# Kernel optimization log

Hardware: AMD Instinct MI355X
Metric: run time of the kernel (lower is better)

Reference implementation:

```python
import jax, jax.numpy as jnp
import numpy as np

B, C, S, H, W = 1, 256, 64, 32, 128
BLOCKS, HEADS, DH = 2, 8, 32
SCALE = DH ** (-0.5)


def layer_norm(x, w, b, eps=1e-5):
    mu = jnp.mean(x, axis=-1, keepdims=True)
    var = jnp.var(x, axis=-1, keepdims=True)
    return (x - mu) * jax.lax.rsqrt(var + eps) * w + b


def generate_y_for_attn(y, u):
    # y: (B,C,H,W), u: (B,S,S) float -> (B, S^2, 2H, C)
    Bv, Cv, Hv, Wv = y.shape
    Sv = u.shape[1]
    uf = jnp.floor(u).reshape(Bv, Sv * Sv)
    u_left = jnp.clip(uf, 0, Wv - 1).astype(jnp.int32)
    u_right = jnp.clip(uf + 1, 0, Wv - 1).astype(jnp.int32)
    yf = y.reshape(Bv, Cv * Hv, Wv)

    def gather_w(idx):
        idxb = jnp.broadcast_to(idx[:, None, :], (Bv, Cv * Hv, Sv * Sv))
        return jnp.take_along_axis(yf, idxb, axis=2).reshape(Bv, Cv, Hv, Sv * Sv)

    ys = jnp.concatenate([gather_w(u_left), gather_w(u_right)], axis=2)  # (B,C,2H,S2)
    return ys.transpose(0, 3, 2, 1)  # (B, S2, 2H, C)


def cross_attention(x, y, p, i):
    # x: (B,M,C), y: (B,M,N,C)
    q = layer_norm(x, p['ln_q_w'][i], p['ln_q_b'][i]) @ p['Wq'][i]        # (B,M,HD)
    k = layer_norm(y, p['ln_k_w'][i], p['ln_k_b'][i]) @ p['Wk'][i]        # (B,M,N,HD)
    v = layer_norm(y, p['ln_v_w'][i], p['ln_v_b'][i]) @ p['Wv'][i]        # (B,M,N,HD)
    Bv, M, _ = q.shape
    N = k.shape[2]
    q = q.reshape(Bv, M, HEADS, DH)
    k = k.reshape(Bv, M, N, HEADS, DH)
    v = v.reshape(Bv, M, N, HEADS, DH)
    dot = SCALE * jnp.einsum('bmhd,bmnhd->bhmn', q, k)                    # (B,H,M,N)
    attn = jax.nn.softmax(dot, axis=-1)
    a = jnp.einsum('bhmn,bmnhd->bmhd', attn, v).reshape(Bv, M, HEADS * DH)
    z = a @ p['Wproj'][i] + p['bproj'][i]
    z = layer_norm(z, p['ln_pre_w'][i], p['ln_pre_b'][i])
    h = jax.nn.gelu(z @ p['Wm1'][i] + p['bm1'][i], approximate=False)
    z = z + (h @ p['Wm2'][i] + p['bm2'][i])
    return layer_norm(z, p['ln_post_w'][i], p['ln_post_b'][i])


def setup_inputs() -> dict:
    key = jax.random.key(0)
    ks = jax.random.split(key, 16)
    std = 0.02
    inp = {
        'grd2sat': jax.random.normal(ks[0], (B, C, S, S), jnp.float32),
        'grd_x': jax.random.normal(ks[1], (B, C, H, W), jnp.float32),
        'u': jax.random.uniform(ks[2], (B, S, S), jnp.float32) * (W - 1),
        'ln_q_w': jnp.ones((BLOCKS, C)), 'ln_q_b': jnp.zeros((BLOCKS, C)),
        'ln_k_w': jnp.ones((BLOCKS, C)), 'ln_k_b': jnp.zeros((BLOCKS, C)),
        'ln_v_w': jnp.ones((BLOCKS, C)), 'ln_v_b': jnp.zeros((BLOCKS, C)),
        'Wq': std * jax.random.normal(ks[3], (BLOCKS, C, HEADS * DH)),
        'Wk': std * jax.random.normal(ks[4], (BLOCKS, C, HEADS * DH)),
        'Wv': std * jax.random.normal(ks[5], (BLOCKS, C, HEADS * DH)),
        'Wproj': std * jax.random.normal(ks[6], (BLOCKS, HEADS * DH, C)),
        'bproj': jnp.zeros((BLOCKS, C)),
        'ln_pre_w': jnp.ones((BLOCKS, C)), 'ln_pre_b': jnp.zeros((BLOCKS, C)),
        'Wm1': std * jax.random.normal(ks[7], (BLOCKS, C, 2 * C)),
        'bm1': jnp.zeros((BLOCKS, 2 * C)),
        'Wm2': std * jax.random.normal(ks[8], (BLOCKS, 2 * C, C)),
        'bm2': jnp.zeros((BLOCKS, C)),
        'ln_post_w': jnp.ones((BLOCKS, C)), 'ln_post_b': jnp.zeros((BLOCKS, C)),
    }
    return inp


def reference(grd2sat, grd_x, u, ln_q_w, ln_q_b, ln_k_w, ln_k_b, ln_v_w, ln_v_b,
              Wq, Wk, Wv, Wproj, bproj, ln_pre_w, ln_pre_b, Wm1, bm1, Wm2, bm2,
              ln_post_w, ln_post_b):
    p = dict(ln_q_w=ln_q_w, ln_q_b=ln_q_b, ln_k_w=ln_k_w, ln_k_b=ln_k_b,
             ln_v_w=ln_v_w, ln_v_b=ln_v_b, Wq=Wq, Wk=Wk, Wv=Wv, Wproj=Wproj,
             bproj=bproj, ln_pre_w=ln_pre_w, ln_pre_b=ln_pre_b, Wm1=Wm1, bm1=bm1,
             Wm2=Wm2, bm2=bm2, ln_post_w=ln_post_w, ln_post_b=ln_post_b)
    y_attn = generate_y_for_attn(grd_x, u)               # (B, S^2, 2H, C)
    x = grd2sat.reshape(B, C, S * S).transpose(0, 2, 1)  # (B, M, C)
    for i in range(BLOCKS):
        # (Swin self-attention layer omitted; cross-attention stack only.)
        x = cross_attention(x, y_attn, p, i)
    out = x.transpose(0, 2, 1).reshape(B, C, S, S)
    # L2 normalize over channel dim
    norm = jnp.sqrt(jnp.sum(out * out, axis=1, keepdims=True))
    return out / jnp.maximum(norm, 1e-12)
```

## Files before the change

kernel.cpp:

```cpp
#include <hip/hip_runtime.h>
#include <math.h>


#define C_DIM 256
#define M_DIM 4096
#define W_DIM 128
#define H_DIM 32
#define ATT_SCALE 0.17677669529663687f

typedef __attribute__((ext_vector_type(8))) short short8;
typedef __attribute__((ext_vector_type(4))) short short4v;
typedef __attribute__((ext_vector_type(4))) float floatx4;

__device__ __forceinline__ unsigned short f2bf(float f) {
    unsigned u = __float_as_uint(f);
    unsigned r = (u + 0x7fffu + ((u >> 16) & 1u)) >> 16;
    return (unsigned short)r;
}
__device__ __forceinline__ float gelu_exact(float x) {
    return 0.5f * x * (1.0f + erff(x * 0.70710678118654752f));
}

struct PrepArgs {
    const float* grd2sat; float* xcur;
    const float* grd_x;   float* yhat;
    const float* u; int* perm; int4* chunks; int* nchunks;
    const float* win[12]; unsigned short* wout[12]; const float* wlnw[12];
    int wR[12], wC[12], wbase[13];
    const float* fW[10]; const float* flnb[10]; const float* fbase[10];
    float* fout[10];
    int fN[10], fwcol[10], focol[10];
};

__global__ __launch_bounds__(256) void prep_kernel(PrepArgs a) {
    __shared__ float smemf[9024];
    int b = blockIdx.x, t = threadIdx.x;
    if (b < 256) {
        float (*tile)[65] = (float(*)[65])smemf;
        int m0 = (b & 63) << 6, c0 = (b >> 6) << 6;
        for (int it = 0; it < 16; ++it) {
            int idx = it * 256 + t;
            int co = idx >> 6, mo = idx & 63;
            tile[co][mo] = a.grd2sat[(size_t)(c0 + co) * M_DIM + m0 + mo];
        }
        __syncthreads();
        for (int it = 0; it < 16; ++it) {
            int idx = it * 256 + t;
            int mo = idx >> 6, co = idx & 63;
// ... 15 lines not shown
        __syncthreads();
        {
            int w = t & 31, part = t >> 5;
            float s = 0.f, ss = 0.f;
            for (int c = part * 32; c < part * 32 + 32; ++c) {
                float x = tile[c][w];
                s += x; ss += x * x;
            }
            ps[part][w] = s; pss[part][w] = ss;
        }
        __syncthreads();
        if (t < 32) {
            float s = 0.f, ss = 0.f;
            for (int p = 0; p < 8; ++p) { s += ps[p][t]; ss += pss[p][t]; }
            float mu = s * (1.f / 256.f);
            float var = ss * (1.f / 256.f) - mu * mu;
            mu_s[t] = mu;
            rs_s[t] = rsqrtf(var + 1e-5f);
        }
        __syncthreads();
        for (int jj = 0; jj < 32; ++jj) {
            float mu = mu_s[jj], rs = rs_s[jj];
            a.yhat[((size_t)(w0 + jj) * H_DIM + h) * C_DIM + t] =
                (tile[t][jj] - mu) * rs;
        }
    } else if (b < 1408) {
        int wI = b - 384;
        int e = 0;
        while (wI >= a.wbase[e + 1]) ++e;
        int tl = wI - a.wbase[e];
        int tilesC = a.wC[e] >> 5;
        int tr = tl / tilesC, tc = tl - tr * tilesC;
        int r0 = tr << 5, c0 = tc << 5;
        const float* in = a.win[e];
        unsigned short* out = a.wout[e];
        const float* lnw = a.wlnw[e];
        int R = a.wR[e], Cc = a.wC[e];
        float (*tile)[33] = (float(*)[33])smemf;
        int rl = t >> 3, cq = (t & 7) << 2;
        float4 v = *(const float4*)&in[(size_t)(r0 + rl) * Cc + c0 + cq];
        if (lnw) {
            float s = lnw[r0 + rl];
            v.x *= s; v.y *= s; v.z *= s; v.w *= s;
        }
        tile[rl][cq + 0] = v.x;
        tile[rl][cq + 1] = v.y;
        tile[rl][cq + 2] = v.z;
        tile[rl][cq + 3] = v.w;
        __syncthreads();
        int cl = t >> 3, rq = (t & 7) << 2;
        ushort4 o;
        o.x = f2bf(tile[rq + 0][cl]);
        o.y = f2bf(tile[rq + 1][cl]);
        o.z = f2bf(tile[rq + 2][cl]);
        o.w = f2bf(tile[rq + 3][cl]);
        *(ushort4*)&out[(size_t)(c0 + cl) * R + r0 + rq] = o;
    } else if (b < 1448) {
        int idx = b - 1408;
        int jj = idx >> 2, part = idx & 3;
        int N = a.fN[jj];
        int c = t & 63, kp = t >> 6;
        int wcol = a.fwcol[jj] + (part << 6) + c;
        const float* W = a.fW[jj];
        const float* lb = a.flnb[jj];
        float s = 0.f;
        for (int k = kp * 64; k < kp * 64 + 64; ++k)
            s += lb[k] * W[(size_t)k * N + wcol];
        smemf[(kp << 6) + c] = s;
        __syncthreads();
        if (t < 64) {
            float tot = smemf[t] + smemf[64 + t] + smemf[128 + t] + smemf[192 + t];
            int ocol = a.focol[jj] + (part << 6) + t;
            if (a.fbase[jj]) tot += a.fbase[jj][a.fwcol[jj] + (part << 6) + t];
            a.fout[jj][ocol] = tot;
        }
    } else {
        int* hist = (int*)smemf;
        int* cur = (int*)smemf + 128;
        unsigned short* wlb = (unsigned short*)((int*)smemf + 256);
        if (t < 128) hist[t] = 0;
        __syncthreads();
        for (int it = 0; it < 16; ++it) {
            int m = it * 256 + t;
            int wl = (int)floorf(a.u[m]);
            wl = max(0, min(wl, 126));
            wlb[m] = (unsigned short)wl;
            atomicAdd(&hist[wl], 1);
        }
// ... 20 lines not shown
            int pos = atomicAdd(&cur[wl], 1);
            a.perm[pos] = m;
        }
    }
}

struct GJ {
    const void* A; const unsigned short* Bt;
    const float* bias;
    void* out; unsigned short* out2;
    int K, N;
};

__device__ __forceinline__ void gemm_core_kv(const GJ& j, short (*As)[264],
                                             short (*Bs)[264], int bm, int by) {
    int t = threadIdx.x;
    int bn = by << 6;
    int wv = t >> 6, lane = t & 63;
    int mt = wv & 1, nt0 = (wv >> 1) << 1;
    int quad = lane >> 4, l16 = lane & 15;
    floatx4 acc0 = {0.f, 0.f, 0.f, 0.f};
    floatx4 acc1 = {0.f, 0.f, 0.f, 0.f};
    {
        int ar = t >> 3, cq = (t & 7) << 2;
        const float* ap = (const float*)j.A + (size_t)(bm + ar) * 256 + cq;
        float4 v[8];
#pragma unroll
        for (int g = 0; g < 8; ++g) v[g] = *(const float4*)(ap + g * 32);
#pragma unroll
        for (int g = 0; g < 8; ++g) {
            short4v o;
            o[0] = (short)f2bf(v[g].x);
            o[1] = (short)f2bf(v[g].y);
            o[2] = (short)f2bf(v[g].z);
            o[3] = (short)f2bf(v[g].w);
            *(short4v*)&As[ar][cq + g * 32] = o;
        }
    }
    {
        int br = t >> 2, cq2 = (t & 3) << 3;
        const unsigned short* bp = j.Bt + (size_t)(bn + br) * 256 + cq2;
#pragma unroll
        for (int g = 0; g < 8; ++g)
            *(short8*)&Bs[br][cq2 + g * 32] = *(const short8*)(bp + g * 32);
    }
    __syncthreads();
#pragma unroll
    for (int k0 = 0; k0 < 8; ++k0) {
        short8 aa = *(const short8*)&As[(mt << 4) + l16][(k0 << 5) + (quad << 3)];
        short8 b0 = *(const short8*)&Bs[(nt0 << 4) + l16][(k0 << 5) + (quad << 3)];
        short8 b1 =
            *(const short8*)&Bs[((nt0 + 1) << 4) + l16][(k0 << 5) + (quad << 3)];
        acc0 = __builtin_amdgcn_mfma_f32_16x16x32_bf16(aa, b0, acc0, 0, 0, 0);
        acc1 = __builtin_amdgcn_mfma_f32_16x16x32_bf16(aa, b1, acc1, 0, 0, 0);
    }
#pragma unroll
    for (int jj = 0; jj < 2; ++jj) {
        const floatx4 accv = jj ? acc1 : acc0;
        int col = bn + ((nt0 + jj) << 4) + l16;
        float bv = j.bias[col];
// ... 12 lines not shown
__global__ __launch_bounds__(256) void kv_kernel(GJ j0, GJ j1) {
    __shared__ short As[32][264];
    __shared__ short Bs[64][264];
    int bm = blockIdx.x << 5;
    if ((int)blockIdx.y < 8)
        gemm_core_kv(j0, As, Bs, bm, blockIdx.y);
    else
        gemm_core_kv(j1, As, Bs, bm, blockIdx.y - 8);
}

struct MegaArgs {
    const float* xcur;
    const int* perm; const int4* chunks; const int* nchunks;
    float* xfinal;
    const unsigned short* Wq[2]; const unsigned short* Wp[2];
    const unsigned short* Wm1[2]; const unsigned short* Wm2[2];
    const unsigned short* Ktb[2]; const unsigned short* Vtb[2];
    const float* qb[2]; const float* m1b[2];
    const float* bpj[2]; const float* bm2v[2];
    const float* pw[2]; const float* pb[2];
    const float* aw; const float* ab;
};

struct BPre { short8 b[8][2]; };

__device__ __forceinline__ void preloadB(const unsigned short* Bt, int Kstride,
                                         int koff, int colw, int l16, int quad,
                                         BPre& P) {
    const unsigned short* bp =
        Bt + (size_t)(colw + l16) * Kstride + koff + (quad << 3);
#pragma unroll
    for (int k0 = 0; k0 < 8; ++k0)
#pragma unroll
        for (int ni = 0; ni < 2; ++ni)
            P.b[k0][ni] =
                *(const short8*)(bp + (size_t)(ni << 4) * Kstride + (k0 << 5));
}

__device__ __forceinline__ void mfma32t(const short* As, int lda, const BPre& P,
                                        int l16, int quad, floatx4 acc[2][2]) {
    const short* ap = As + (size_t)l16 * lda + (quad << 3);
#pragma unroll
    for (int k0 = 0; k0 < 8; ++k0) {
        short8 a0 = *(const short8*)(ap + (k0 << 5));
        short8 a1 = *(const short8*)(ap + (size_t)16 * lda + (k0 << 5));
        acc[0][0] = __builtin_amdgcn_mfma_f32_16x16x32_bf16(a0, P.b[k0][0], acc[0][0], 0, 0, 0);
        acc[0][1] = __builtin_amdgcn_mfma_f32_16x16x32_bf16(a0, P.b[k0][1], acc[0][1], 0, 0, 0);
        acc[1][0] = __builtin_amdgcn_mfma_f32_16x16x32_bf16(a1, P.b[k0][0], acc[1][0], 0, 0, 0);
        acc[1][1] = __builtin_amdgcn_mfma_f32_16x16x32_bf16(a1, P.b[k0][1], acc[1][1], 0, 0, 0);
    }
}

#define ZACC(A) \
    { A[0][0] = (floatx4){0.f,0.f,0.f,0.f}; A[0][1] = (floatx4){0.f,0.f,0.f,0.f}; \
      A[1][0] = (floatx4){0.f,0.f,0.f,0.f}; A[1][1] = (floatx4){0.f,0.f,0.f,0.f}; }

__global__ __launch_bounds__(512) void mega_kernel(MegaArgs a) {
    __shared__ __align__(16) char smem[137856];
    short (*XH)[264] = (short(*)[264])(smem);
    short (*QR)[264] = (short(*)[264])(smem + 16896);
    short (*ZH)[264] = (short(*)[264])(smem + 33792);
    short (*AR)[264] = (short(*)[264])(smem + 50688);
    float (*Zf)[260] = (float(*)[260])(smem + 67584);
    short (*PB)[32][72] = (short(*)[32][72])(smem + 100864);
    int* gp = (int*)(smem + 137728);

    if ((int)blockIdx.x >= *a.nchunks) return;
    int4 cd = a.chunks[blockIdx.x];
    int wl = cd.x, qstart = cd.y, qcnt = cd.z;
    int t = threadIdx.x;
    if (t < 32) gp[t] = (t < qcnt) ? a.perm[qstart + t] : a.perm[qstart];
    __syncthreads();

    int wv = t >> 6, lane = t & 63, quad = lane >> 4, l16 = lane & 15;
    int colw = wv << 5;
    int r16 = t >> 4, c0 = (t & 15) << 4;

#pragma unroll 1
    for (int l = 0; l < 2; ++l) {
        BPre Pq;
        preloadB(a.Wq[l], 256, 0, colw, l16, quad, Pq);
        {
            float4 v[4];
            if (l == 0) {
                const float* xp = a.xcur + (size_t)gp[r16] * 256 + c0;
#pragma unroll
                for (int g4 = 0; g4 < 4; ++g4)
                    v[g4] = *(const float4*)(xp + (g4 << 2));
            } else {
#pragma unroll
                for (int g4 = 0; g4 < 4; ++g4)
                    v[g4] = *(const float4*)&Zf[r16][c0 + (g4 << 2)];
            }
            float s = 0.f, ss = 0.f;
#pragma unroll
            for (int g4 = 0; g4 < 4; ++g4) {
                s += v[g4].x + v[g4].y + v[g4].z + v[g4].w;
                ss += v[g4].x * v[g4].x + v[g4].y * v[g4].y + v[g4].z * v[g4].z +
                      v[g4].w * v[g4].w;
            }
#pragma unroll
            for (int o = 1; o < 16; o <<= 1) {
                s += __shfl_xor(s, o, 64);
                ss += __shfl_xor(ss, o, 64);
            }
            float mu = s * (1.f / 256.f);
            float rs = rsqrtf(ss * (1.f / 256.f) - mu * mu + 1e-5f);
#pragma unroll
            for (int g4 = 0; g4 < 4; ++g4) {
                v[g4].x = (v[g4].x - mu) * rs;
                v[g4].y = (v[g4].y - mu) * rs;
                v[g4].z = (v[g4].z - mu) * rs;
                v[g4].w = (v[g4].w - mu) * rs;
            }
            if (l == 1) {
                float s2 = 0.f, ss2 = 0.f;
#pragma unroll
                for (int g4 = 0; g4 < 4; ++g4) {
                    float4 w4 = *(const float4*)&a.aw[c0 + (g4 << 2)];
                    float4 b4 = *(const float4*)&a.ab[c0 + (g4 << 2)];
                    v[g4].x = v[g4].x * w4.x + b4.x;
                    v[g4].y = v[g4].y * w4.y + b4.y;
                    v[g4].z = v[g4].z * w4.z + b4.z;
                    v[g4].w = v[g4].w * w4.w + b4.w;
                    s2 += v[g4].x + v[g4].y + v[g4].z + v[g4].w;
                    ss2 += v[g4].x * v[g4].x + v[g4].y * v[g4].y +
                           v[g4].z * v[g4].z + v[g4].w * v[g4].w;
                }
#pragma unroll
                for (int o = 1; o < 16; o <<= 1) {
                    s2 += __shfl_xor(s2, o, 64);
                    ss2 += __shfl_xor(ss2, o, 64);
                }
                float mu2 = s2 * (1.f / 256.f);
                float rs2 = rsqrtf(ss2 * (1.f / 256.f) - mu2 * mu2 + 1e-5f);
#pragma unroll
                for (int g4 = 0; g4 < 4; ++g4) {
                    v[g4].x = (v[g4].x - mu2) * rs2;
                    v[g4].y = (v[g4].y - mu2) * rs2;
                    v[g4].z = (v[g4].z - mu2) * rs2;
                    v[g4].w = (v[g4].w - mu2) * rs2;
                }
            }
#pragma unroll
            for (int g4 = 0; g4 < 4; ++g4) {
                short4v o;
                o[0] = (short)f2bf(v[g4].x);
                o[1] = (short)f2bf(v[g4].y);
                o[2] = (short)f2bf(v[g4].z);
                o[3] = (short)f2bf(v[g4].w);
                *(short4v*)&XH[r16][c0 + (g4 << 2)] = o;
            }
        }
        __syncthreads();

        short8 kb[4], vfrag[2][2];
        {
            const unsigned short* Kt = a.Ktb[l];
            const unsigned short* Vt = a.Vtb[l];
            int h = wv;
#pragma unroll
            for (int nt = 0; nt < 4; ++nt)
                kb[nt] = *(const short8*)(
                    Kt + (size_t)((wl << 5) + (nt << 4) + l16) * 256 +
                    (h << 5) + (quad << 3));
#pragma unroll
            for (int ks = 0; ks < 2; ++ks)
#pragma unroll
                for (int dt = 0; dt < 2; ++dt)
                    vfrag[ks][dt] = *(const short8*)(
                        Vt + (size_t)((h << 5) + (dt << 4) + l16) * M_DIM +
                        (wl << 5) + (ks << 5) + (quad << 3));
        }
        {
            floatx4 acc[2][2];
            ZACC(acc);
            mfma32t((const short*)XH, 264, Pq, l16, quad, acc);
            const float* qb = a.qb[l];
#pragma unroll
            for (int ni = 0; ni < 2; ++ni) {
                int col = colw + (ni << 4) + l16;
                float bv = qb[col];
#pragma unroll
                for (int mi = 0; mi < 2; ++mi)
#pragma unroll
                    for (int r = 0; r < 4; ++r)
                        QR[(mi << 4) + (quad << 2) + r][col] =
                            (short)f2bf(acc[mi][ni][r] + bv);
            }
        }
        __syncthreads();

        BPre Pp;
        {
            int h = wv;
            short8 aq0 = *(const short8*)&QR[l16][(h << 5) + (quad << 3)];
            short8 aq1 = *(const short8*)&QR[16 + l16][(h << 5) + (quad << 3)];
            floatx4 c[2][4];
#pragma unroll
            for (int nt = 0; nt < 4; ++nt) {
                floatx4 z = {0.f, 0.f, 0.f, 0.f};
                c[0][nt] = __builtin_amdgcn_mfma_f32_16x16x32_bf16(aq0, kb[nt], z, 0, 0, 0);
                c[1][nt] = __builtin_amdgcn_mfma_f32_16x16x32_bf16(aq1, kb[nt], z, 0, 0, 0);
            }
            floatx4 ri[2];
#pragma unroll
            for (int m = 0; m < 2; ++m) {
#pragma unroll
                for (int nt = 0; nt < 4; ++nt) {
                    floatx4 e;
#pragma unroll
                    for (int r = 0; r < 4; ++r)
                        e[r] = __expf(c[m][nt][r] * ATT_SCALE);
                    c[m][nt] = e;
                }
                floatx4 s4 = c[m][0] + c[m][1] + c[m][2] + c[m][3];
#pragma unroll
                for (int r = 0; r < 4; ++r) {
                    float s = s4[r];
                    s += __shfl_xor(s, 1, 64);
                    s += __shfl_xor(s, 2, 64);
                    s += __shfl_xor(s, 4, 64);
                    s += __shfl_xor(s, 8, 64);
                    ri[m][r] = 1.f / s;
                }
            }
#pragma unroll
            for (int m = 0; m < 2; ++m)
#pragma unroll
                for (int nt = 0; nt < 4; ++nt)
#pragma unroll
                    for (int r = 0; r < 4; ++r)
                        PB[wv][(m << 4) + (quad << 2) + r][(nt << 4) + l16] =
                            (short)f2bf(c[m][nt][r] * ri[m][r]);
            __threadfence_block();
            preloadB(a.Wp[l], 256, 0, colw, l16, quad, Pp);
            floatx4 o[2][2];
#pragma unroll
            for (int m = 0; m < 2; ++m)
#pragma unroll
                for (int dt = 0; dt < 2; ++dt)
                    o[m][dt] = (floatx4){0.f, 0.f, 0.f, 0.f};
#pragma unroll
            for (int ks = 0; ks < 2; ++ks) {
                short8 pa0 =
                    *(const short8*)&PB[wv][l16][(ks << 5) + (quad << 3)];
                short8 pa1 =
                    *(const short8*)&PB[wv][16 + l16][(ks << 5) + (quad << 3)];
#pragma unroll
                for (int dt = 0; dt < 2; ++dt) {
                    o[0][dt] = __builtin_amdgcn_mfma_f32_16x16x32_bf16(
                        pa0, vfrag[ks][dt], o[0][dt], 0, 0, 0);
                    o[1][dt] = __builtin_amdgcn_mfma_f32_16x16x32_bf16(
                        pa1, vfrag[ks][dt], o[1][dt], 0, 0, 0);
                }
            }
            int h5 = wv << 5;
#pragma unroll
            for (int m = 0; m < 2; ++m)
#pragma unroll
                for (int dt = 0; dt < 2; ++dt)
#pragma unroll
                    for (int r = 0; r < 4; ++r)
                        AR[(m << 4) + (quad << 2) + r]
                          [h5 + (dt << 4) + l16] = (short)f2bf(o[m][dt][r]);
        }
        __syncthreads();

        {
            floatx4 acc[2][2];
            ZACC(acc);
            mfma32t((const short*)AR, 264, Pp, l16, quad, acc);
            const float* bpj = a.bpj[l];
#pragma unroll
            for (int ni = 0; ni < 2; ++ni) {
                int col = colw + (ni << 4) + l16;
                float bv = bpj[col];
#pragma unroll
                for (int mi = 0; mi < 2; ++mi)
#pragma unroll
                    for (int r = 0; r < 4; ++r)
                        Zf[(mi << 4) + (quad << 2) + r][col] = acc[mi][ni][r] + bv;
            }
        }
        __syncthreads();

        BPre Pm1a;
        preloadB(a.Wm1[l], 256, 0, colw, l16, quad, Pm1a);
        {
            const float* pw = a.pw[l];
            const float* pb = a.pb[l];
            float4 v[4];
#pragma unroll
            for (int g4 = 0; g4 < 4; ++g4)
                v[g4] = *(const float4*)&Zf[r16][c0 + (g4 << 2)];
            float s = 0.f, ss = 0.f;
#pragma unroll
            for (int g4 = 0; g4 < 4; ++g4) {
                s += v[g4].x + v[g4].y + v[g4].z + v[g4].w;
                ss += v[g4].x * v[g4].x + v[g4].y * v[g4].y + v[g4].z * v[g4].z +
                      v[g4].w * v[g4].w;
            }
#pragma unroll
            for (int o = 1; o < 16; o <<= 1) {
                s += __shfl_xor(s, o, 64);
                ss += __shfl_xor(ss, o, 64);
            }
            float mu = s * (1.f / 256.f);
            float rs = rsqrtf(ss * (1.f / 256.f) - mu * mu + 1e-5f);
#pragma unroll
            for (int g4 = 0; g4 < 4; ++g4) {
                float4 z;
                z.x = (v[g4].x - mu) * rs;
                z.y = (v[g4].y - mu) * rs;
                z.z = (v[g4].z - mu) * rs;
                z.w = (v[g4].w - mu) * rs;
                short4v o;
                o[0] = (short)f2bf(z.x);
                o[1] = (short)f2bf(z.y);
                o[2] = (short)f2bf(z.z);
                o[3] = (short)f2bf(z.w);
                *(short4v*)&ZH[r16][c0 + (g4 << 2)] = o;
                float4 w4 = *(const float4*)&pw[c0 + (g4 << 2)];
                float4 b4 = *(const float4*)&pb[c0 + (g4 << 2)];
                float4 za;
                za.x = z.x * w4.x + b4.x;
                za.y = z.y * w4.y + b4.y;
                za.z = z.z * w4.z + b4.z;
                za.w = z.w * w4.w + b4.w;
                *(float4*)&Zf[r16][c0 + (g4 << 2)] = za;
            }
        }
        __syncthreads();

        const float* m1b = a.m1b[l];
        BPre Pm2a;
        {
            floatx4 acc[2][2];
            ZACC(acc);
            mfma32t((const short*)ZH, 264, Pm1a, l16, quad, acc);
            BPre Pm1b;
            preloadB(a.Wm1[l] + (size_t)256 * 256, 256, 0, colw, l16, quad, Pm1b);
#pragma unroll
            for (int ni = 0; ni < 2; ++ni) {
                int col = colw + (ni << 4) + l16;
                float bv = m1b[col];
#pragma unroll
                for (int mi = 0; mi < 2; ++mi)
#pragma unroll
                    for (int r = 0; r < 4; ++r)
                        XH[(mi << 4) + (quad << 2) + r][col] =
                            (short)f2bf(gelu_exact(acc[mi][ni][r] + bv));
            }
            floatx4 acc2[2][2];
            ZACC(acc2);
            mfma32t((const short*)ZH, 264, Pm1b, l16, quad, acc2);
            preloadB(a.Wm2[l], 512, 0, colw, l16, quad, Pm2a);
#pragma unroll
            for (int ni = 0; ni < 2; ++ni) {
                int col = colw + (ni << 4) + l16;
                float bv = m1b[256 + col];
#pragma unroll
                for (int mi = 0; mi < 2; ++mi)
#pragma unroll
                    for (int r = 0; r < 4; ++r)
                        QR[(mi << 4) + (quad << 2) + r][col] =
                            (short)f2bf(gelu_exact(acc2[mi][ni][r] + bv));
            }
        }
        __syncthreads();

        {
            floatx4 macc[2][2];
            ZACC(macc);
            mfma32t((const short*)XH, 264, Pm2a, l16, quad, macc);
            BPre Pm2b;
            preloadB(a.Wm2[l], 512, 256, colw, l16, quad, Pm2b);
            mfma32t((const short*)QR, 264, Pm2b, l16, quad, macc);
            const float* b2 = a.bm2v[l];
#pragma unroll
            for (int ni = 0; ni < 2; ++ni) {
                int col = colw + (ni << 4) + l16;
                float bv = b2[col];
#pragma unroll
                for (int mi = 0; mi < 2; ++mi)
#pragma unroll
                    for (int r = 0; r < 4; ++r) {
                        int row = (mi << 4) + (quad << 2) + r;
                        float v = macc[mi][ni][r] + bv + Zf[row][col];
                        if (l == 0) {
                            Zf[row][col] = v;
                        } else if (row < qcnt) {
                            a.xfinal[(size_t)gp[row] * 256 + col] = v;
                        }
                    }
            }
        }
        __syncthreads();
    }
}

__global__ __launch_bounds__(256) void out_kernel(const float* __restrict__ X,
                                                  const float* __restrict__ w,
                                                  const float* __restrict__ b,
                                                  float* __restrict__ out) {
    __shared__ float tile[64][65];
    int t = threadIdx.x;
    int mo = t >> 2, q = t & 3;
    int m0 = blockIdx.x << 6;
    const float* p = X + (size_t)(m0 + mo) * C_DIM + (q << 6);
    float4 v[16];
    float s = 0.f, ss = 0.f;
#pragma unroll
    for (int c = 0; c < 16; ++c) {
        v[c] = *(const float4*)(p + c * 4);
        s += v[c].x + v[c].y + v[c].z + v[c].w;
        ss += v[c].x * v[c].x + v[c].y * v[c].y + v[c].z * v[c].z + v[c].w * v[c].w;
    }
    s += __shfl_xor(s, 1, 64); s += __shfl_xor(s, 2, 64);
    ss += __shfl_xor(ss, 1, 64); ss += __shfl_xor(ss, 2, 64);
    float mu = s * (1.f / 256.f);
    float rs = rsqrtf(ss * (1.f / 256.f) - mu * mu + 1e-5f);
    float ss2 = 0.f;
#pragma unroll
    for (int c = 0; c < 16; ++c) {
        float4 w4 = *(const float4*)&w[(q << 6) + c * 4];
        float4 b4 = *(const float4*)&b[(q << 6) + c * 4];
        v[c].x = (v[c].x - mu) * rs * w4.x + b4.x;
        v[c].y = (v[c].y - mu) * rs * w4.y + b4.y;
        v[c].z = (v[c].z - mu) * rs * w4.z + b4.z;
        v[c].w = (v[c].w - mu) * rs * w4.w + b4.w;
        ss2 += v[c].x * v[c].x + v[c].y * v[c].y + v[c].z * v[c].z + v[c].w * v[c].w;
    }
    ss2 += __shfl_xor(ss2, 1, 64); ss2 += __shfl_xor(ss2, 2, 64);
    float sc = 1.f / fmaxf(sqrtf(ss2), 1e-12f);
    for (int cc = 0; cc < 4; ++cc) {
        if (q == cc) {
#pragma unroll
            for (int c = 0; c < 16; ++c) {
                tile[mo][c * 4 + 0] = v[c].x * sc;
                tile[mo][c * 4 + 1] = v[c].y * sc;
                tile[mo][c * 4 + 2] = v[c].z * sc;
                tile[mo][c * 4 + 3] = v[c].w * sc;
            }
        }
        __syncthreads();
        for (int it = 0; it < 16; ++it) {
            int idx = it * 256 + t;
            int co = idx >> 6, mr = idx & 63;
            out[(size_t)((cc << 6) + co) * M_DIM + m0 + mr] = tile[mr][co];
        }
        __syncthreads();
    }
}

extern "C" void kernel_launch(void* const* d_in, const int* in_sizes, int n_in,
                              void* d_out, int out_size, void* d_ws, size_t ws_size,
                              hipStream_t stream) {
    const float* grd2sat = (const float*)d_in[0];
    const float* grd_x   = (const float*)d_in[1];
    const float* u       = (const float*)d_in[2];
    const float* ln_q_w  = (const float*)d_in[3];
    const float* ln_q_b  = (const float*)d_in[4];
    const float* ln_k_w  = (const float*)d_in[5];
    const float* ln_k_b  = (const float*)d_in[6];
    const float* ln_v_w  = (const float*)d_in[7];
    const float* ln_v_b  = (const float*)d_in[8];
    const float* Wq      = (const float*)d_in[9];
    const float* Wk      = (const float*)d_in[10];
    const float* Wv      = (const float*)d_in[11];
    const float* Wproj   = (const float*)d_in[12];
    const float* bproj   = (const float*)d_in[13];
    const float* ln_pre_w = (const float*)d_in[14];
    const float* ln_pre_b = (const float*)d_in[15];
    const float* Wm1     = (const float*)d_in[16];
    const float* bm1     = (const float*)d_in[17];
    const float* Wm2     = (const float*)d_in[18];
    const float* bm2     = (const float*)d_in[19];
    const float* ln_post_w = (const float*)d_in[20];
    const float* ln_post_b = (const float*)d_in[21];

    float* ws   = (float*)d_ws;
    float* yhat = ws;
    float* xcur = ws + 1048576;
    float* zq   = ws + 2097152;
    unsigned short* Ktab0 = (unsigned short*)(ws + 6291456);
    unsigned short* Vt0   = (unsigned short*)(ws + 6815744);
    unsigned short* Ktab1 = (unsigned short*)(ws + 7340032);
    unsigned short* Vt1   = (unsigned short*)(ws + 7864320);
    unsigned short* Bt    = (unsigned short*)(ws + 8388608);
    float* biasbuf = ws + 8912896;
    int*  perm    = (int*)(ws + 8915456);
    int4* chunks  = (int4*)(ws + 8919552);
    int*  nchunks = (int*)(ws + 8921600);
    const size_t BS = 524288;
    const size_t OQ = 0, OKV = 65536, OP = 196608, OM1 = 262144, OM2 = 393216;

    dim3 b256(256);

    PrepArgs pa;
    pa.grd2sat = grd2sat; pa.xcur = xcur;
    pa.grd_x = grd_x;     pa.yhat = yhat;
    pa.u = u; pa.perm = perm; pa.chunks = chunks; pa.nchunks = nchunks;
    {
        int base = 0;
        for (int i = 0; i < 2; ++i) {
// ... 43 lines not shown
    jkv0.A = yhat; jkv0.Bt = Bt + OKV; jkv0.bias = biasbuf + 256;
    jkv0.out = Ktab0; jkv0.out2 = Vt0; jkv0.K = 256; jkv0.N = 512;
    GJ jkv1 = {};
    jkv1.A = yhat; jkv1.Bt = Bt + BS + OKV; jkv1.bias = biasbuf + 1280 + 256;
    jkv1.out = Ktab1; jkv1.out2 = Vt1; jkv1.K = 256; jkv1.N = 512;
    kv_kernel<<<dim3(128, 16), b256, 0, stream>>>(jkv0, jkv1);

    MegaArgs ma;
    ma.xcur = xcur; ma.perm = perm; ma.chunks = chunks; ma.nchunks = nchunks;
    ma.xfinal = zq;
    for (int i = 0; i < 2; ++i) {
        const unsigned short* bt = Bt + i * BS;
        ma.Wq[i] = bt + OQ; ma.Wp[i] = bt + OP;
        ma.Wm1[i] = bt + OM1; ma.Wm2[i] = bt + OM2;
        ma.Ktb[i] = i ? Ktab1 : Ktab0; ma.Vtb[i] = i ? Vt1 : Vt0;
        ma.qb[i] = biasbuf + i * 1280;
        ma.m1b[i] = biasbuf + i * 1280 + 768;
        ma.bpj[i] = bproj + i * 256;
        ma.bm2v[i] = bm2 + i * 256;
        ma.pw[i] = ln_pre_w + i * 256;
        ma.pb[i] = ln_pre_b + i * 256;
    }
    ma.aw = ln_post_w; ma.ab = ln_post_b;
    mega_kernel<<<288, dim3(512), 0, stream>>>(ma);

    out_kernel<<<64, b256, 0, stream>>>(zq, ln_post_w + 256, ln_post_b + 256,
                                        (float*)d_out);
}
```

Baseline: 207.1 us.

## Double mega kernel threads, store yhat in bf16, retile out kernel

Raises the fused per-chunk kernel from 512 to 1024 threads so each wave owns 16 output columns and half a head's rows, shrinking per-wave register footprint and raising parallelism. Stores the normalized y tensor as bf16 so the K/V projection kernel loads bf16 directly instead of converting fp32. Retiles the output normalization kernel to 32 rows per block with a single transpose pass and more blocks, and adds an unroll pragma in the prep bias fold. Risks include higher register pressure limits at 1024 threads and a slight precision change on yhat.

Measured after the change: 206.6 us. About the same (-0.2%).

```diff
diff --git a/kernel.cpp b/kernel.cpp
--- a/kernel.cpp
+++ b/kernel.cpp
@@ -23,7 +23,7 @@
 
 struct PrepArgs {
     const float* grd2sat; float* xcur;
-    const float* grd_x;   float* yhat;
+    const float* grd_x;   unsigned short* yhat;
     const float* u; int* perm; int4* chunks; int* nchunks;
     const float* win[12]; unsigned short* wout[12]; const float* wlnw[12];
     int wR[12], wC[12], wbase[13];
@@ -85,7 +85,7 @@
         for (int jj = 0; jj < 32; ++jj) {
             float mu = mu_s[jj], rs = rs_s[jj];
             a.yhat[((size_t)(w0 + jj) * H_DIM + h) * C_DIM + t] =
-                (tile[t][jj] - mu) * rs;
+                f2bf((tile[t][jj] - mu) * rs);
         }
     } else if (b < 1408) {
         int wI = b - 384;
@@ -127,6 +127,7 @@
         const float* W = a.fW[jj];
         const float* lb = a.flnb[jj];
         float s = 0.f;
+#pragma unroll 4
         for (int k = kp * 64; k < kp * 64 + 64; ++k)
             s += lb[k] * W[(size_t)k * N + wcol];
         smemf[(kp << 6) + c] = s;
@@ -193,20 +194,12 @@
     floatx4 acc0 = {0.f, 0.f, 0.f, 0.f};
     floatx4 acc1 = {0.f, 0.f, 0.f, 0.f};
     {
-        int ar = t >> 3, cq = (t & 7) << 2;
-        const float* ap = (const float*)j.A + (size_t)(bm + ar) * 256 + cq;
-        float4 v[8];
-#pragma unroll
-        for (int g = 0; g < 8; ++g) v[g] = *(const float4*)(ap + g * 32);
-#pragma unroll
-        for (int g = 0; g < 8; ++g) {
-            short4v o;
-            o[0] = (short)f2bf(v[g].x);
-            o[1] = (short)f2bf(v[g].y);
-            o[2] = (short)f2bf(v[g].z);
-            o[3] = (short)f2bf(v[g].w);
-            *(short4v*)&As[ar][cq + g * 32] = o;
-        }
+        int ar = t >> 3, cq = (t & 7) << 5;
+        const unsigned short* ap =
+            (const unsigned short*)j.A + (size_t)(bm + ar) * 256 + cq;
+#pragma unroll
+        for (int c = 0; c < 4; ++c)
+            *(uint4*)&As[ar][cq + (c << 3)] = *(const uint4*)(ap + (c << 3));
     }
     {
         int br = t >> 2, cq2 = (t & 3) << 3;
@@ -265,23 +258,39 @@
     const float* aw; const float* ab;
 };
 
-struct BPre { short8 b[8][2]; };
-
-__device__ __forceinline__ void preloadB(const unsigned short* Bt, int Kstride,
+struct BPre8 { short8 b[8]; };
+struct BPre16 { short8 b[8][2]; };
+
+__device__ __forceinline__ void preload8(const unsigned short* Bt, int Ks,
                                          int koff, int colw, int l16, int quad,
-                                         BPre& P) {
-    const unsigned short* bp =
-        Bt + (size_t)(colw + l16) * Kstride + koff + (quad << 3);
+                                         BPre8& P) {
+    const unsigned short* bp = Bt + (size_t)(colw + l16) * Ks + koff + (quad << 3);
+#pragma unroll
+    for (int k0 = 0; k0 < 8; ++k0) P.b[k0] = *(const short8*)(bp + (k0 << 5));
+}
+__device__ __forceinline__ void preload16(const unsigned short* Bt, int Ks,
+                                          int colw, int l16, int quad, BPre16& P) {
+    const unsigned short* bp = Bt + (size_t)(colw + l16) * Ks + (quad << 3);
 #pragma unroll
     for (int k0 = 0; k0 < 8; ++k0)
 #pragma unroll
-        for (int ni = 0; ni < 2; ++ni)
-            P.b[k0][ni] =
-                *(const short8*)(bp + (size_t)(ni << 4) * Kstride + (k0 << 5));
-}
-
-__device__ __forceinline__ void mfma32t(const short* As, int lda, const BPre& P,
-                                        int l16, int quad, floatx4 acc[2][2]) {
+        for (int nt = 0; nt < 2; ++nt)
+            P.b[k0][nt] = *(const short8*)(bp + (size_t)(nt << 4) * Ks + (k0 << 5));
+}
+
+__device__ __forceinline__ void mfma16(const short* As, int lda, const BPre8& P,
+                                       int l16, int quad, floatx4 acc[2]) {
+    const short* ap = As + (size_t)l16 * lda + (quad << 3);
+#pragma unroll
+    for (int k0 = 0; k0 < 8; ++k0) {
+        short8 a0 = *(const short8*)(ap + (k0 << 5));
+        short8 a1 = *(const short8*)(ap + (size_t)16 * lda + (k0 << 5));
+        acc[0] = __builtin_amdgcn_mfma_f32_16x16x32_bf16(a0, P.b[k0], acc[0], 0, 0, 0);
+        acc[1] = __builtin_amdgcn_mfma_f32_16x16x32_bf16(a1, P.b[k0], acc[1], 0, 0, 0);
+    }
+}
+__device__ __forceinline__ void mfma16x2(const short* As, int lda, const BPre16& P,
+                                         int l16, int quad, floatx4 acc[2][2]) {
     const short* ap = As + (size_t)l16 * lda + (quad << 3);
 #pragma unroll
     for (int k0 = 0; k0 < 8; ++k0) {
@@ -294,18 +303,14 @@
     }
 }
 
-#define ZACC(A) \
-    { A[0][0] = (floatx4){0.f,0.f,0.f,0.f}; A[0][1] = (floatx4){0.f,0.f,0.f,0.f}; \
-      A[1][0] = (floatx4){0.f,0.f,0.f,0.f}; A[1][1] = (floatx4){0.f,0.f,0.f,0.f}; }
-
-__global__ __launch_bounds__(512) void mega_kernel(MegaArgs a) {
+__global__ __launch_bounds__(1024) void mega_kernel(MegaArgs a) {
     __shared__ __align__(16) char smem[137856];
     short (*XH)[264] = (short(*)[264])(smem);
     short (*QR)[264] = (short(*)[264])(smem + 16896);
     short (*ZH)[264] = (short(*)[264])(smem + 33792);
     short (*AR)[264] = (short(*)[264])(smem + 50688);
     float (*Zf)[260] = (float(*)[260])(smem + 67584);
-    short (*PB)[32][72] = (short(*)[32][72])(smem + 100864);
+    short (*PB)[16][72] = (short(*)[16][72])(smem + 100864);
     int* gp = (int*)(smem + 137728);
 
     if ((int)blockIdx.x >= *a.nchunks) return;
@@ -316,83 +321,82 @@
     __syncthreads();
 
     int wv = t >> 6, lane = t & 63, quad = lane >> 4, l16 = lane & 15;
-    int colw = wv << 5;
-    int r16 = t >> 4, c0 = (t & 15) << 4;
+    int colw = wv << 4;
+    int colw2 = wv << 5;
+    int r32 = t >> 5, c8 = (t & 31) << 3;
 
 #pragma unroll 1
     for (int l = 0; l < 2; ++l) {
-        BPre Pq;
-        preloadB(a.Wq[l], 256, 0, colw, l16, quad, Pq);
-        {
-            float4 v[4];
+        BPre8 Pq;
+        preload8(a.Wq[l], 256, 0, colw, l16, quad, Pq);
+        {
+            float4 v[2];
             if (l == 0) {
-                const float* xp = a.xcur + (size_t)gp[r16] * 256 + c0;
-#pragma unroll
-                for (int g4 = 0; g4 < 4; ++g4)
-                    v[g4] = *(const float4*)(xp + (g4 << 2));
+                const float* xp = a.xcur + (size_t)gp[r32] * 256 + c8;
+                v[0] = *(const float4*)(xp);
+                v[1] = *(const float4*)(xp + 4);
             } else {
-#pragma unroll
-                for (int g4 = 0; g4 < 4; ++g4)
-                    v[g4] = *(const float4*)&Zf[r16][c0 + (g4 << 2)];
+                v[0] = *(const float4*)&Zf[r32][c8];
+                v[1] = *(const float4*)&Zf[r32][c8 + 4];
             }
             float s = 0.f, ss = 0.f;
 #pragma unroll
-            for (int g4 = 0; g4 < 4; ++g4) {
-                s += v[g4].x + v[g4].y + v[g4].z + v[g4].w;
-                ss += v[g4].x * v[g4].x + v[g4].y * v[g4].y + v[g4].z * v[g4].z +
-                      v[g4].w * v[g4].w;
-            }
-#pragma unroll
-            for (int o = 1; o < 16; o <<= 1) {
+            for (int g = 0; g < 2; ++g) {
+                s += v[g].x + v[g].y + v[g].z + v[g].w;
+                ss += v[g].x * v[g].x + v[g].y * v[g].y + v[g].z * v[g].z +
+                      v[g].w * v[g].w;
+            }
+#pragma unroll
+            for (int o = 1; o < 32; o <<= 1) {
                 s += __shfl_xor(s, o, 64);
                 ss += __shfl_xor(ss, o, 64);
             }
             float mu = s * (1.f / 256.f);
             float rs = rsqrtf(ss * (1.f / 256.f) - mu * mu + 1e-5f);
 #pragma unroll
-            for (int g4 = 0; g4 < 4; ++g4) {
-                v[g4].x = (v[g4].x - mu) * rs;
-                v[g4].y = (v[g4].y - mu) * rs;
-                v[g4].z = (v[g4].z - mu) * rs;
-                v[g4].w = (v[g4].w - mu) * rs;
+            for (int g = 0; g < 2; ++g) {
+                v[g].x = (v[g].x - mu) * rs;
+                v[g].y = (v[g].y - mu) * rs;
+                v[g].z = (v[g].z - mu) * rs;
+                v[g].w = (v[g].w - mu) * rs;
             }
             if (l == 1) {
                 float s2 = 0.f, ss2 = 0.f;
 #pragma unroll
-                for (int g4 = 0; g4 < 4; ++g4) {
-                    float4 w4 = *(const float4*)&a.aw[c0 + (g4 << 2)];
-                    float4 b4 = *(const float4*)&a.ab[c0 + (g4 << 2)];
-                    v[g4].x = v[g4].x * w4.x + b4.x;
-                    v[g4].y = v[g4].y * w4.y + b4.y;
-                    v[g4].z = v[g4].z * w4.z + b4.z;
-                    v[g4].w = v[g4].w * w4.w + b4.w;
-                    s2 += v[g4].x + v[g4].y + v[g4].z + v[g4].w;
-                    ss2 += v[g4].x * v[g4].x + v[g4].y * v[g4].y +
-                           v[g4].z * v[g4].z + v[g4].w * v[g4].w;
+                for (int g = 0; g < 2; ++g) {
+                    float4 w4 = *(const float4*)&a.aw[c8 + (g << 2)];
+                    float4 b4 = *(const float4*)&a.ab[c8 + (g << 2)];
+                    v[g].x = v[g].x * w4.x + b4.x;
+                    v[g].y = v[g].y * w4.y + b4.y;
+                    v[g].z = v[g].z * w4.z + b4.z;
+                    v[g].w = v[g].w * w4.w + b4.w;
+                    s2 += v[g].x + v[g].y + v[g].z + v[g].w;
+                    ss2 += v[g].x * v[g].x + v[g].y * v[g].y + v[g].z * v[g].z +
+                           v[g].w * v[g].w;
                 }
 #pragma unroll
-                for (int o = 1; o < 16; o <<= 1) {
+                for (int o = 1; o < 32; o <<= 1) {
                     s2 += __shfl_xor(s2, o, 64);
                     ss2 += __shfl_xor(ss2, o, 64);
                 }
                 float mu2 = s2 * (1.f / 256.f);
                 float rs2 = rsqrtf(ss2 * (1.f / 256.f) - mu2 * mu2 + 1e-5f);
 #pragma unroll
-                for (int g4 = 0; g4 < 4; ++g4) {
-                    v[g4].x = (v[g4].x - mu2) * rs2;
-                    v[g4].y = (v[g4].y - mu2) * rs2;
-                    v[g4].z = (v[g4].z - mu2) * rs2;
-                    v[g4].w = (v[g4].w - mu2) * rs2;
+                for (int g = 0; g < 2; ++g) {
+                    v[g].x = (v[g].x - mu2) * rs2;
+                    v[g].y = (v[g].y - mu2) * rs2;
+                    v[g].z = (v[g].z - mu2) * rs2;
+                    v[g].w = (v[g].w - mu2) * rs2;
                 }
             }
 #pragma unroll
-            for (int g4 = 0; g4 < 4; ++g4) {
+            for (int g = 0; g < 2; ++g) {
                 short4v o;
-                o[0] = (short)f2bf(v[g4].x);
-                o[1] = (short)f2bf(v[g4].y);
-                o[2] = (short)f2bf(v[g4].z);
-                o[3] = (short)f2bf(v[g4].w);
-                *(short4v*)&XH[r16][c0 + (g4 << 2)] = o;
+                o[0] = (short)f2bf(v[g].x);
+                o[1] = (short)f2bf(v[g].y);
+                o[2] = (short)f2bf(v[g].z);
+                o[3] = (short)f2bf(v[g].w);
+                *(short4v*)&XH[r32][c8 + (g << 2)] = o;
             }
         }
         __syncthreads();
@@ -401,7 +405,7 @@
         {
             const unsigned short* Kt = a.Ktb[l];
             const unsigned short* Vt = a.Vtb[l];
-            int h = wv;
+            int h = wv >> 1;
 #pragma unroll
             for (int nt = 0; nt < 4; ++nt)
                 kb[nt] = *(const short8*)(
@@ -416,228 +420,187 @@
                         (wl << 5) + (ks << 5) + (quad << 3));
         }
         {
-            floatx4 acc[2][2];
-            ZACC(acc);
-            mfma32t((const short*)XH, 264, Pq, l16, quad, acc);
-            const float* qb = a.qb[l];
-#pragma unroll
-            for (int ni = 0; ni < 2; ++ni) {
-                int col = colw + (ni << 4) + l16;
-                float bv = qb[col];
-#pragma unroll
-                for (int mi = 0; mi < 2; ++mi)
-#pragma unroll
-                    for (int r = 0; r < 4; ++r)
-                        QR[(mi << 4) + (quad << 2) + r][col] =
-                            (short)f2bf(acc[mi][ni][r] + bv);
-            }
-        }
-        __syncthreads();
-
-        BPre Pp;
-        {
-            int h = wv;
-            short8 aq0 = *(const short8*)&QR[l16][(h << 5) + (quad << 3)];
-            short8 aq1 = *(const short8*)&QR[16 + l16][(h << 5) + (quad << 3)];
-            floatx4 c[2][4];
+            floatx4 acc[2];
+            acc[0] = (floatx4){0.f, 0.f, 0.f, 0.f};
+            acc[1] = (floatx4){0.f, 0.f, 0.f, 0.f};
+            mfma16((const short*)XH, 264, Pq, l16, quad, acc);
+            int col = colw + l16;
+            float bv = a.qb[l][col];
+#pragma unroll
+            for (int mi = 0; mi < 2; ++mi)
+#pragma unroll
+                for (int r = 0; r < 4; ++r)
+                    QR[(mi << 4) + (quad << 2) + r][col] =
+                        (short)f2bf(acc[mi][r] + bv);
+        }
+        __syncthreads();
+
+        BPre8 Pp;
+        {
+            int h = wv >> 1, mh = wv & 1;
+            short8 aq = *(const short8*)&QR[(mh << 4) + l16][(h << 5) + (quad << 3)];
+            floatx4 c[4];
 #pragma unroll
             for (int nt = 0; nt < 4; ++nt) {
                 floatx4 z = {0.f, 0.f, 0.f, 0.f};
-                c[0][nt] = __builtin_amdgcn_mfma_f32_16x16x32_bf16(aq0, kb[nt], z, 0, 0, 0);
-                c[1][nt] = __builtin_amdgcn_mfma_f32_16x16x32_bf16(aq1, kb[nt], z, 0, 0, 0);
-            }
-            floatx4 ri[2];
-#pragma unroll
-            for (int m = 0; m < 2; ++m) {
-#pragma unroll
-                for (int nt = 0; nt < 4; ++nt) {
-                    floatx4 e;
-#pragma unroll
-                    for (int r = 0; r < 4; ++r)
-                        e[r] = __expf(c[m][nt][r] * ATT_SCALE);
-                    c[m][nt] = e;
-                }
-                floatx4 s4 = c[m][0] + c[m][1] + c[m][2] + c[m][3];
-#pragma unroll
-                for (int r = 0; r < 4; ++r) {
-                    float s = s4[r];
-                    s += __shfl_xor(s, 1, 64);
-                    s += __shfl_xor(s, 2, 64);
-                    s += __shfl_xor(s, 4, 64);
-                    s += __shfl_xor(s, 8, 64);
-                    ri[m][r] = 1.f / s;
-                }
-            }
-#pragma unroll
-            for (int m = 0; m < 2; ++m)
-#pragma unroll
-                for (int nt = 0; nt < 4; ++nt)
-#pragma unroll
-                    for (int r = 0; r < 4; ++r)
-                        PB[wv][(m << 4) + (quad << 2) + r][(nt << 4) + l16] =
-                            (short)f2bf(c[m][nt][r] * ri[m][r]);
+                c[nt] = __builtin_amdgcn_mfma_f32_16x16x32_bf16(aq, kb[nt], z, 0, 0, 0);
+            }
+#pragma unroll
+            for (int nt = 0; nt < 4; ++nt) {
+                floatx4 e;
+#pragma unroll
+                for (int r = 0; r < 4; ++r) e[r] = __expf(c[nt][r] * ATT_SCALE);
+                c[nt] = e;
+            }
+            floatx4 s4 = c[0] + c[1] + c[2] + c[3];
+            floatx4 ri;
+#pragma unroll
+            for (int r = 0; r < 4; ++r) {
+                float s = s4[r];
+                s += __shfl_xor(s, 1, 64);
+                s += __shfl_xor(s, 2, 64);
+                s += __shfl_xor(s, 4, 64);
+                s += __shfl_xor(s, 8, 64);
+                ri[r] = 1.f / s;
+            }
+#pragma unroll
+            for (int nt = 0; nt < 4; ++nt)
+#pragma unroll
+                for (int r = 0; r < 4; ++r)
+                    PB[wv][(quad << 2) + r][(nt << 4) + l16] =
+                        (short)f2bf(c[nt][r] * ri[r]);
             __threadfence_block();
-            preloadB(a.Wp[l], 256, 0, colw, l16, quad, Pp);
-            floatx4 o[2][2];
-#pragma unroll
-            for (int m = 0; m < 2; ++m)
+            preload8(a.Wp[l], 256, 0, colw, l16, quad, Pp);
+            floatx4 o[2];
+            o[0] = (floatx4){0.f, 0.f, 0.f, 0.f};
+            o[1] = (floatx4){0.f, 0.f, 0.f, 0.f};
+#pragma unroll
+            for (int ks = 0; ks < 2; ++ks) {
+                short8 pa = *(const short8*)&PB[wv][l16][(ks << 5) + (quad << 3)];
 #pragma unroll
                 for (int dt = 0; dt < 2; ++dt)
-                    o[m][dt] = (floatx4){0.f, 0.f, 0.f, 0.f};
-#pragma unroll
-            for (int ks = 0; ks < 2; ++ks) {
-                short8 pa0 =
-                    *(const short8*)&PB[wv][l16][(ks << 5) + (quad << 3)];
-                short8 pa1 =
-                    *(const short8*)&PB[wv][16 + l16][(ks << 5) + (quad << 3)];
-#pragma unroll
-                for (int dt = 0; dt < 2; ++dt) {
-                    o[0][dt] = __builtin_amdgcn_mfma_f32_16x16x32_bf16(
-                        pa0, vfrag[ks][dt], o[0][dt], 0, 0, 0);
-                    o[1][dt] = __builtin_amdgcn_mfma_f32_16x16x32_bf16(
-                        pa1, vfrag[ks][dt], o[1][dt], 0, 0, 0);
-                }
-            }
-            int h5 = wv << 5;
-#pragma unroll
-            for (int m = 0; m < 2; ++m)
-#pragma unroll
-                for (int dt = 0; dt < 2; ++dt)
-#pragma unroll
-                    for (int r = 0; r < 4; ++r)
-                        AR[(m << 4) + (quad << 2) + r]
-                          [h5 + (dt << 4) + l16] = (short)f2bf(o[m][dt][r]);
-        }
-        __syncthreads();
-
-        {
-            floatx4 acc[2][2];
-            ZACC(acc);
-            mfma32t((const short*)AR, 264, Pp, l16, quad, acc);
-            const float* bpj = a.bpj[l];
-#pragma unroll
-            for (int ni = 0; ni < 2; ++ni) {
-                int col = colw + (ni << 4) + l16;
-                float bv = bpj[col];
-#pragma unroll
-                for (int mi = 0; mi < 2; ++mi)
-#pragma unroll
-                    for (int r = 0; r < 4; ++r)
-                        Zf[(mi << 4) + (quad << 2) + r][col] = acc[mi][ni][r] + bv;
-            }
-        }
-        __syncthreads();
-
-        BPre Pm1a;
-        preloadB(a.Wm1[l], 256, 0, colw, l16, quad, Pm1a);
+                    o[dt] = __builtin_amdgcn_mfma_f32_16x16x32_bf16(
+                        pa, vfrag[ks][dt], o[dt], 0, 0, 0);
+            }
+#pragma unroll
+            for (int dt = 0; dt < 2; ++dt)
+#pragma unroll
+                for (int r = 0; r < 4; ++r)
+                    AR[(mh << 4) + (quad << 2) + r]
+                      [(h << 5) + (dt << 4) + l16] = (short)f2bf(o[dt][r]);
+        }
+        __syncthreads();
+
+        {
+            floatx4 acc[2];
+            acc[0] = (floatx4){0.f, 0.f, 0.f, 0.f};
+            acc[1] = (floatx4){0.f, 0.f, 0.f, 0.f};
+            mfma16((const short*)AR, 264, Pp, l16, quad, acc);
+            int col = colw + l16;
+            float bv = a.bpj[l][col];
+#pragma unroll
+            for (int mi = 0; mi < 2; ++mi)
+#pragma unroll
+                for (int r = 0; r < 4; ++r)
+                    Zf[(mi << 4) + (quad << 2) + r][col] = acc[mi][r] + bv;
+        }
+        __syncthreads();
+
+        BPre16 Pm1;
+        preload16(a.Wm1[l], 256, colw2, l16, quad, Pm1);
         {
             const float* pw = a.pw[l];
             const float* pb = a.pb[l];
-            float4 v[4];
-#pragma unroll
-            for (int g4 = 0; g4 < 4; ++g4)
-                v[g4] = *(const float4*)&Zf[r16][c0 + (g4 << 2)];
+            float4 v[2];
+            v[0] = *(const float4*)&Zf[r32][c8];
+            v[1] = *(const float4*)&Zf[r32][c8 + 4];
             float s = 0.f, ss = 0.f;
 #pragma unroll
-            for (int g4 = 0; g4 < 4; ++g4) {
-                s += v[g4].x + v[g4].y + v[g4].z + v[g4].w;
-                ss += v[g4].x * v[g4].x + v[g4].y * v[g4].y + v[g4].z * v[g4].z +
-                      v[g4].w * v[g4].w;
-            }
-#pragma unroll
-            for (int o = 1; o < 16; o <<= 1) {
+            for (int g = 0; g < 2; ++g) {
+                s += v[g].x + v[g].y + v[g].z + v[g].w;
+                ss += v[g].x * v[g].x + v[g].y * v[g].y + v[g].z * v[g].z +
+                      v[g].w * v[g].w;
+            }
+#pragma unroll
+            for (int o = 1; o < 32; o <<= 1) {
                 s += __shfl_xor(s, o, 64);
                 ss += __shfl_xor(ss, o, 64);
             }
             float mu = s * (1.f / 256.f);
             float rs = rsqrtf(ss * (1.f / 256.f) - mu * mu + 1e-5f);
 #pragma unroll
-            for (int g4 = 0; g4 < 4; ++g4) {
+            for (int g = 0; g < 2; ++g) {
                 float4 z;
-                z.x = (v[g4].x - mu) * rs;
-                z.y = (v[g4].y - mu) * rs;
-                z.z = (v[g4].z - mu) * rs;
-                z.w = (v[g4].w - mu) * rs;
+                z.x = (v[g].x - mu) * rs;
+                z.y = (v[g].y - mu) * rs;
+                z.z = (v[g].z - mu) * rs;
+                z.w = (v[g].w - mu) * rs;
                 short4v o;
                 o[0] = (short)f2bf(z.x);
                 o[1] = (short)f2bf(z.y);
                 o[2] = (short)f2bf(z.z);
                 o[3] = (short)f2bf(z.w);
-                *(short4v*)&ZH[r16][c0 + (g4 << 2)] = o;
-                float4 w4 = *(const float4*)&pw[c0 + (g4 << 2)];
-                float4 b4 = *(const float4*)&pb[c0 + (g4 << 2)];
+                *(short4v*)&ZH[r32][c8 + (g << 2)] = o;
+                float4 w4 = *(const float4*)&pw[c8 + (g << 2)];
+                float4 b4 = *(const float4*)&pb[c8 + (g << 2)];
                 float4 za;
                 za.x = z.x * w4.x + b4.x;
                 za.y = z.y * w4.y + b4.y;
                 za.z = z.z * w4.z + b4.z;
                 za.w = z.w * w4.w + b4.w;
-                *(float4*)&Zf[r16][c0 + (g4 << 2)] = za;
-            }
-        }
-        __syncthreads();
-
-        const float* m1b = a.m1b[l];
-        BPre Pm2a;
-        {
-            floatx4 acc[2][2];
-            ZACC(acc);
-            mfma32t((const short*)ZH, 264, Pm1a, l16, quad, acc);
-            BPre Pm1b;
-            preloadB(a.Wm1[l] + (size_t)256 * 256, 256, 0, colw, l16, quad, Pm1b);
-#pragma unroll
-            for (int ni = 0; ni < 2; ++ni) {
-                int col = colw + (ni << 4) + l16;
+                *(float4*)&Zf[r32][c8 + (g << 2)] = za;
+            }
+        }
+        __syncthreads();
+
+        BPre8 Pm2a;
+        {
+            floatx4 acc2[2][2];
+            acc2[0][0] = (floatx4){0.f, 0.f, 0.f, 0.f};
+            acc2[0][1] = (floatx4){0.f, 0.f, 0.f, 0.f};
+            acc2[1][0] = (floatx4){0.f, 0.f, 0.f, 0.f};
+            acc2[1][1] = (floatx4){0.f, 0.f, 0.f, 0.f};
+            mfma16x2((const short*)ZH, 264, Pm1, l16, quad, acc2);
+            preload8(a.Wm2[l], 512, 0, colw, l16, quad, Pm2a);
+            const float* m1b = a.m1b[l];
+#pragma unroll
+            for (int nt = 0; nt < 2; ++nt) {
+                int col = colw2 + (nt << 4) + l16;
                 float bv = m1b[col];
+                short (*H)[264] = (col >> 8) ? QR : XH;
+                int lc = col & 255;
 #pragma unroll
                 for (int mi = 0; mi < 2; ++mi)
 #pragma unroll
                     for (int r = 0; r < 4; ++r)
-                        XH[(mi << 4) + (quad << 2) + r][col] =
-                            (short)f2bf(gelu_exact(acc[mi][ni][r] + bv));
-            }
-            floatx4 acc2[2][2];
-            ZACC(acc2);
-            mfma32t((const short*)ZH, 264, Pm1b, l16, quad, acc2);
-            preloadB(a.Wm2[l], 512, 0, colw, l16, quad, Pm2a);
-#pragma unroll
-            for (int ni = 0; ni < 2; ++ni) {
-                int col = colw + (ni << 4) + l16;
-                float bv = m1b[256 + col];
-#pragma unroll
-                for (int mi = 0; mi < 2; ++mi)
-#pragma unroll
-                    for (int r = 0; r < 4; ++r)
-                        QR[(mi << 4) + (quad << 2) + r][col] =
-                            (short)f2bf(gelu_exact(acc2[mi][ni][r] + bv));
-            }
-        }
-        __syncthreads();
-
-        {
-            floatx4 macc[2][2];
-            ZACC(macc);
-            mfma32t((const short*)XH, 264, Pm2a, l16, quad, macc);
-            BPre Pm2b;
-            preloadB(a.Wm2[l], 512, 256, colw, l16, quad, Pm2b);
-            mfma32t((const short*)QR, 264, Pm2b, l16, quad, macc);
-            const float* b2 = a.bm2v[l];
-#pragma unroll
-            for (int ni = 0; ni < 2; ++ni) {
-                int col = colw + (ni << 4) + l16;
-                float bv = b2[col];
-#pragma unroll
-                for (int mi = 0; mi < 2; ++mi)
-#pragma unroll
-                    for (int r = 0; r < 4; ++r) {
-                        int row = (mi << 4) + (quad << 2) + r;
-                        float v = macc[mi][ni][r] + bv + Zf[row][col];
-                        if (l == 0) {
-                            Zf[row][col] = v;
-                        } else if (row < qcnt) {
-                            a.xfinal[(size_t)gp[row] * 256 + col] = v;
-                        }
+                        H[(mi << 4) + (quad << 2) + r][lc] =
+                            (short)f2bf(gelu_exact(acc2[mi][nt][r] + bv));
+            }
+        }
+        __syncthreads();
+
+        {
+            floatx4 macc[2];
+            macc[0] = (floatx4){0.f, 0.f, 0.f, 0.f};
+            macc[1] = (floatx4){0.f, 0.f, 0.f, 0.f};
+            mfma16((const short*)XH, 264, Pm2a, l16, quad, macc);
+            BPre8 Pm2b;
+            preload8(a.Wm2[l], 512, 256, colw, l16, quad, Pm2b);
+            mfma16((const short*)QR, 264, Pm2b, l16, quad, macc);
+            int col = colw + l16;
+            float bv = a.bm2v[l][col];
+#pragma unroll
+            for (int mi = 0; mi < 2; ++mi)
+#pragma unroll
+                for (int r = 0; r < 4; ++r) {
+                    int row = (mi << 4) + (quad << 2) + r;
+                    float v = macc[mi][r] + bv + Zf[row][col];
+                    if (l == 0) {
+                        Zf[row][col] = v;
+                    } else if (row < qcnt) {
+                        a.xfinal[(size_t)gp[row] * 256 + col] = v;
                     }
-            }
+                }
         }
         __syncthreads();
     }
@@ -647,53 +610,49 @@
                                                   const float* __restrict__ w,
                                                   const float* __restrict__ b,
                                                   float* __restrict__ out) {
-    __shared__ float tile[64][65];
+    __shared__ float tile[32][261];
     int t = threadIdx.x;
-    int mo = t >> 2, q = t & 3;
-    int m0 = blockIdx.x << 6;
-    const float* p = X + (size_t)(m0 + mo) * C_DIM + (q << 6);
-    float4 v[16];
+    int mo = t >> 3, q = t & 7;
+    int m0 = blockIdx.x << 5;
+    const float* p = X + (size_t)(m0 + mo) * C_DIM + (q << 5);
+    float4 v[8];
     float s = 0.f, ss = 0.f;
 #pragma unroll
-    for (int c = 0; c < 16; ++c) {
+    for (int c = 0; c < 8; ++c) {
         v[c] = *(const float4*)(p + c * 4);
         s += v[c].x + v[c].y + v[c].z + v[c].w;
         ss += v[c].x * v[c].x + v[c].y * v[c].y + v[c].z * v[c].z + v[c].w * v[c].w;
     }
-    s += __shfl_xor(s, 1, 64); s += __shfl_xor(s, 2, 64);
-    ss += __shfl_xor(ss, 1, 64); ss += __shfl_xor(ss, 2, 64);
+    s += __shfl_xor(s, 1, 64); s += __shfl_xor(s, 2, 64); s += __shfl_xor(s, 4, 64);
+    ss += __shfl_xor(ss, 1, 64); ss += __shfl_xor(ss, 2, 64); ss += __shfl_xor(ss, 4, 64);
     float mu = s * (1.f / 256.f);
     float rs = rsqrtf(ss * (1.f / 256.f) - mu * mu + 1e-5f);
     float ss2 = 0.f;
 #pragma unroll
-    for (int c = 0; c < 16; ++c) {
-        float4 w4 = *(const float4*)&w[(q << 6) + c * 4];
-        float4 b4 = *(const float4*)&b[(q << 6) + c * 4];
+    for (int c = 0; c < 8; ++c) {
+        float4 w4 = *(const float4*)&w[(q << 5) + c * 4];
+        float4 b4 = *(const float4*)&b[(q << 5) + c * 4];
         v[c].x = (v[c].x - mu) * rs * w4.x + b4.x;
         v[c].y = (v[c].y - mu) * rs * w4.y + b4.y;
         v[c].z = (v[c].z - mu) * rs * w4.z + b4.z;
         v[c].w = (v[c].w - mu) * rs * w4.w + b4.w;
         ss2 += v[c].x * v[c].x + v[c].y * v[c].y + v[c].z * v[c].z + v[c].w * v[c].w;
     }
-    ss2 += __shfl_xor(ss2, 1, 64); ss2 += __shfl_xor(ss2, 2, 64);
+    ss2 += __shfl_xor(ss2, 1, 64); ss2 += __shfl_xor(ss2, 2, 64); ss2 += __shfl_xor(ss2, 4, 64);
     float sc = 1.f / fmaxf(sqrtf(ss2), 1e-12f);
-    for (int cc = 0; cc < 4; ++cc) {
-        if (q == cc) {
-#pragma unroll
-            for (int c = 0; c < 16; ++c) {
-                tile[mo][c * 4 + 0] = v[c].x * sc;
-                tile[mo][c * 4 + 1] = v[c].y * sc;
-                tile[mo][c * 4 + 2] = v[c].z * sc;
-                tile[mo][c * 4 + 3] = v[c].w * sc;
-            }
-        }
-        __syncthreads();
-        for (int it = 0; it < 16; ++it) {
-            int idx = it * 256 + t;
-            int co = idx >> 6, mr = idx & 63;
-            out[(size_t)((cc << 6) + co) * M_DIM + m0 + mr] = tile[mr][co];
-        }
-        __syncthreads();
+#pragma unroll
+    for (int c = 0; c < 8; ++c) {
+        tile[mo][(q << 5) + c * 4 + 0] = v[c].x * sc;
+        tile[mo][(q << 5) + c * 4 + 1] = v[c].y * sc;
+        tile[mo][(q << 5) + c * 4 + 2] = v[c].z * sc;
+        tile[mo][(q << 5) + c * 4 + 3] = v[c].w * sc;
+    }
+    __syncthreads();
+#pragma unroll 1
+    for (int it = 0; it < 32; ++it) {
+        int idx = it * 256 + t;
+        int c = idx >> 5, m = idx & 31;
+        out[(size_t)c * M_DIM + m0 + m] = tile[m][c];
     }
 }
 
@@ -724,7 +683,7 @@
     const float* ln_post_b = (const float*)d_in[21];
 
     float* ws   = (float*)d_ws;
-    float* yhat = ws;
+    unsigned short* yhat = (unsigned short*)ws;
     float* xcur = ws + 1048576;
     float* zq   = ws + 2097152;
     unsigned short* Ktab0 = (unsigned short*)(ws + 6291456);
@@ -814,8 +773,8 @@
         ma.pb[i] = ln_pre_b + i * 256;
     }
     ma.aw = ln_post_w; ma.ab = ln_post_b;
-    mega_kernel<<<288, dim3(512), 0, stream>>>(ma);
-
-    out_kernel<<<64, b256, 0, stream>>>(zq, ln_post_w + 256, ln_post_b + 256,
-                                        (float*)d_out);
-}
+    mega_kernel<<<288, dim3(1024), 0, stream>>>(ma);
+
+    out_kernel<<<128, b256, 0, stream>>>(zq, ln_post_w + 256, ln_post_b + 256,
+                                         (float*)d_out);
+}
```
